# Kernel optimization log

Hardware: AMD Instinct MI355X
Metric: run time of the kernel (lower is better)

The kernel has to match this reference:

```python
import jax, jax.numpy as jnp
import numpy as np

GRID = (8, 8)
B, C, H, W = 16, 256, 64, 64
N_NETS = GRID[0] * GRID[1]
EPS = 1e-5  # torch BatchNorm2d default


def _region_index():
    # Faithful to the original code: networks[i * j + j] == networks[j*(i+1)]
    gh, gw = GRID
    i = np.arange(gh)[:, None]
    j = np.arange(gw)[None, :]
    return (i * j + j).reshape(-1)  # [gh*gw] int indices into the 64 networks


def setup_inputs() -> dict:
    key = jax.random.key(0)
    ks = jax.random.split(key, 7)
    x = jax.random.normal(ks[0], (B, C, H, W), jnp.float32)
    gamma = 1.0 + 0.1 * jax.random.normal(ks[1], (N_NETS, C), jnp.float32)
    beta = 0.1 * jax.random.normal(ks[2], (N_NETS, C), jnp.float32)
    mean = 0.1 * jax.random.normal(ks[3], (N_NETS, C), jnp.float32)
    var = jax.random.uniform(ks[4], (N_NETS, C), jnp.float32, minval=0.5, maxval=1.5)
    conv_w = 0.05 * jax.random.normal(ks[5], (N_NETS, C, C, 3, 3), jnp.float32)
    conv_b = 0.01 * jax.random.normal(ks[6], (N_NETS, C), jnp.float32)
    return dict(x=x, gamma=gamma, beta=beta, mean=mean, var=var,
                conv_w=conv_w, conv_b=conv_b)


def reference(x, gamma, beta, mean, var, conv_w, conv_b):
    gh, gw = GRID
    b, c, h, w = x.shape
    ph, pw = h // gh, w // gw
    # [B,C,H,W] -> [gh*gw, B, C, ph, pw]
    xp = (x.reshape(b, c, gh, ph, gw, pw)
           .transpose(2, 4, 0, 1, 3, 5)
           .reshape(gh * gw, b, c, ph, pw))

    idx = jnp.asarray(_region_index())
    g, bt, m, v = gamma[idx], beta[idx], mean[idx], var[idx]
    wk, cb = conv_w[idx], conv_b[idx]

    def region(xi, gi, bi, mi, vi, wi, cbi):
        # inference-mode BatchNorm2d
        scale = (gi * jax.lax.rsqrt(vi + EPS))[None, :, None, None]
        hh = (xi - mi[None, :, None, None]) * scale + bi[None, :, None, None]
        hh = jax.nn.relu(hh)
        y = jax.lax.conv_general_dilated(
            hh, wi, window_strides=(1, 1), padding=((1, 1), (1, 1)),
            dimension_numbers=('NCHW', 'OIHW', 'NCHW'))
        return y + cbi[None, :, None, None] + xi  # residual add

    yp = jax.vmap(region)(xp, g, bt, m, v, wk, cb)  # [gh*gw, B, C, ph, pw]
    y = (yp.reshape(gh, gw, b, c, ph, pw)
           .transpose(2, 3, 0, 4, 1, 5)
           .reshape(b, c, h, w))
    return y
```

## Files before the change

### kernel.cpp

```cpp
#include <hip/hip_runtime.h>
#include <hip/hip_bf16.h>
#include <stdint.h>


typedef __attribute__((ext_vector_type(8))) short bf16x8;
typedef __attribute__((ext_vector_type(4))) float f32x4;

typedef const __attribute__((address_space(1))) unsigned int gu32;
typedef __attribute__((address_space(3))) unsigned int lu32;

__device__ __forceinline__ void g2l16(const void* g, void* l) {
  __builtin_amdgcn_global_load_lds((gu32*)g, (lu32*)l, 16, 0, 0);
}

__device__ __forceinline__ unsigned short f2bf(float f) {
  union { __hip_bfloat16 h; unsigned short u; } cv;
  cv.h = __float2bfloat16(f);
  return cv.u;
}

__global__ void wtrans_kernel(const float* __restrict__ w,
                              __hip_bfloat16* __restrict__ wb) {
  const int co8 = blockIdx.x;
  const int net = blockIdx.y;
  const int tid = threadIdx.x;
  __shared__ __align__(16) unsigned short t[9 * 8 * 256];

  const int cip = tid & 127;
  const int ch  = tid >> 7;
  const int ci0 = cip * 2;

#pragma unroll
  for (int cl = 0; cl < 4; ++cl) {
    const int col = ch * 4 + cl;
    const int co = co8 * 8 + col;
    const float* src = w + ((size_t)(net * 256 + co) * 256 + ci0) * 9;
    float a[18];
#pragma unroll
    for (int i = 0; i < 18; ++i) a[i] = src[i];
#pragma unroll
    for (int tap = 0; tap < 9; ++tap) {
      unsigned int pk = (unsigned)f2bf(a[tap]) | ((unsigned)f2bf(a[tap + 9]) << 16);
      *(unsigned int*)&t[tap * 2048 + col * 256 + ci0] = pk;
    }
  }
  __syncthreads();

  __hip_bfloat16* base = wb + (size_t)net * 589824;
#pragma unroll
  for (int k = 0; k < 9; ++k) {
    int ck = k * 256 + tid;
    int tap = ck >> 8;
    int col = (ck >> 5) & 7;
    int cr = ck & 31;
    bf16x8 v = *(const bf16x8*)&t[tap * 2048 + col * 256 + cr * 8];
    unsigned short* dst = (unsigned short*)base +
        ((size_t)tap * 256 + co8 * 8 + col) * 256 + cr * 8;
    *(bf16x8*)dst = v;
  }
}

__global__ void bnrelu_kernel(const float* __restrict__ x,
                              const float* __restrict__ gamma,
                              const float* __restrict__ beta,
                              const float* __restrict__ mean,
                              const float* __restrict__ var,
                              __hip_bfloat16* __restrict__ hh) {
  const int blk = blockIdx.x;
  const int reg = blk >> 4, b = blk & 15;
  const int gi = reg >> 3, gj = reg & 7;
  const int net = gj * (gi + 1);
  const int tid = threadIdx.x;

  __shared__ float sc[256], sh[256];
  __shared__ __align__(16) unsigned short tile[64 * 256];

  {
    float g = gamma[net * 256 + tid];
    float bt = beta[net * 256 + tid];
    float m = mean[net * 256 + tid];
    float v = var[net * 256 + tid];
    float s = g * rsqrtf(v + 1e-5f);
    sc[tid] = s;
    sh[tid] = bt - m * s;
  }
  __syncthreads();

  const float* xb = x + (size_t)b * 1048576 + (gi * 8) * 64 + gj * 8;
  const int px = tid & 63, cw = tid >> 6;
  const int yy = px >> 3, xx = px & 7;

#pragma unroll
  for (int j = 0; j < 8; ++j) {
    const int chunk = cw * 8 + j;
    const int c0 = chunk * 8;
    bf16x8 v;
#pragma unroll
    for (int e = 0; e < 8; ++e) {
      int c = c0 + e;
      float tv = xb[(size_t)c * 4096 + yy * 64 + xx];
      tv = fmaxf(tv * sc[c] + sh[c], 0.f);
      v[e] = (short)f2bf(tv);
    }
    int phys = (chunk + px) & 31;
    *(bf16x8*)&tile[px * 256 + phys * 8] = v;
  }
  __syncthreads();

  unsigned short* hb = (unsigned short*)(hh + (size_t)(reg * 16 + b) * 16384);
#pragma unroll
  for (int k = 0; k < 8; ++k) {
    int ck = k * 256 + tid;
    int p = ck >> 5, cl = ck & 31;
    int phys = (cl + p) & 31;
    bf16x8 v = *(const bf16x8*)&tile[p * 256 + phys * 8];
    *(bf16x8*)(hb + p * 256 + cl * 8) = v;
  }
}

__global__ __launch_bounds__(256, 2) void conv_kernel(
    const __hip_bfloat16* __restrict__ hh,
    const __hip_bfloat16* __restrict__ wb,
    const float* __restrict__ xin,
    const float* __restrict__ cbias,
    float* __restrict__ outp) {
  __shared__ __align__(16) char sA[66048];

  const int bx = blockIdx.x;
  const int r = bx >> 4;
  const int mt = bx & 7;
  const int nt = (bx >> 3) & 1;
  const int gi = r >> 3, gj = r & 7;
  const int net = gj * (gi + 1);

  const int tid = threadIdx.x;
  const int lane = tid & 63;
  const int wv = tid >> 6;
  const int wm = (wv & 1) * 64;
  const int wn = (wv >> 1) * 64;
  const int ln = lane & 15;
  const int q = lane >> 4;

  const __hip_bfloat16* Aslab = hh + (size_t)(r * 16 + mt * 2) * (64 * 256);

#pragma unroll
  for (int i = 0; i < 16; ++i) {
    int s = i * 256 + tid;
    int row = s >> 5, sp = s & 31;
    int cl = (sp & 24) | (((sp & 7) - row) & 7);
    g2l16(Aslab + (size_t)row * 256 + cl * 8, sA + s * 16);
  }
  if (tid < 32) *(f32x4*)(sA + 65536 + tid * 16) = (f32x4){0.f, 0.f, 0.f, 0.f};
  __syncthreads();

  const unsigned short* Bl = (const unsigned short*)wb +
      (size_t)net * 589824 + (size_t)(nt * 128 + wn + ln) * 256 + q * 8;

  int bl[4], py[4], pxr[4];
#pragma unroll
  for (int mf = 0; mf < 4; ++mf) {
    int m = wm + mf * 16 + ln;
    bl[mf] = m >> 6;
    py[mf] = (m >> 3) & 7;
    pxr[mf] = m & 7;
  }

  f32x4 acc[4][4];
#pragma unroll
  for (int mf = 0; mf < 4; ++mf)
#pragma unroll
    for (int nf = 0; nf < 4; ++nf)
      acc[mf][nf] = (f32x4){0.f, 0.f, 0.f, 0.f};

#pragma unroll 1
  for (int cc = 0; cc < 4; ++cc) {
#pragma unroll
    for (int tap = 0; tap < 9; ++tap) {
      const int dy = tap / 3 - 1, dx = tap % 3 - 1;
      bf16x8 bfr[4][2];
#pragma unroll
      for (int nf = 0; nf < 4; ++nf)
#pragma unroll
        for (int kk = 0; kk < 2; ++kk)
          bfr[nf][kk] = *(const bf16x8*)(Bl + (size_t)tap * 65536 +
                                         nf * 4096 + cc * 64 + kk * 32);
      int arow[4];
#pragma unroll
      for (int mf = 0; mf < 4; ++mf) {
        int sy = py[mf] + dy, sx = pxr[mf] + dx;
        bool v = ((unsigned)sy < 8u) & ((unsigned)sx < 8u);
        arow[mf] = v ? (bl[mf] * 64 + sy * 8 + sx) : 128;
      }
#pragma unroll
      for (int kk = 0; kk < 2; ++kk) {
        bf16x8 afr[4];
#pragma unroll
        for (int mf = 0; mf < 4; ++mf) {
          int row = arow[mf];
          int phys = cc * 8 + ((kk * 4 + q + row) & 7);
          afr[mf] = *(const bf16x8*)(sA + row * 512 + phys * 16);
        }
#pragma unroll
        for (int mf = 0; mf < 4; ++mf)
#pragma unroll
          for (int nf = 0; nf < 4; ++nf)
            acc[mf][nf] = __builtin_amdgcn_mfma_f32_16x16x32_bf16(
                afr[mf], bfr[nf][kk], acc[mf][nf], 0, 0, 0);
      }
    }
  }

  const int nbase = nt * 128 + wn;
#pragma unroll
  for (int nf = 0; nf < 4; ++nf) {
    const int n = nbase + nf * 16 + ln;
    const float cb = cbias[net * 256 + n];
#pragma unroll
    for (int mf = 0; mf < 4; ++mf) {
      int mloc = wm + mf * 16 + q * 4;
      int b = mt * 2 + (mloc >> 6);
      int px = mloc & 63;
      int yy = px >> 3, x0 = px & 7;
      size_t off =
          (((size_t)b * 256 + n) * 64 + (gi * 8 + yy)) * 64 + (gj * 8 + x0);
      f32x4 res = *(const f32x4*)(xin + off);
      f32x4 o = acc[mf][nf];
      o = o + res;
      o = o + cb;
      *(f32x4*)(outp + off) = o;
    }
  }
}

extern "C" void kernel_launch(void* const* d_in, const int* in_sizes, int n_in,
                              void* d_out, int out_size, void* d_ws,
                              size_t ws_size, hipStream_t stream) {
  const float* x      = (const float*)d_in[0];
  const float* gamma  = (const float*)d_in[1];
  const float* beta   = (const float*)d_in[2];
  const float* mean   = (const float*)d_in[3];
  const float* var    = (const float*)d_in[4];
  const float* conv_w = (const float*)d_in[5];
  const float* conv_b = (const float*)d_in[6];
  float* out = (float*)d_out;

  __hip_bfloat16* wb = (__hip_bfloat16*)d_ws;
  __hip_bfloat16* hh = (__hip_bfloat16*)((char*)d_ws + 75497472);

  wtrans_kernel<<<dim3(32, 64), 256, 0, stream>>>(conv_w, wb);
  bnrelu_kernel<<<1024, 256, 0, stream>>>(x, gamma, beta, mean, var, hh);
  conv_kernel<<<1024, 256, 0, stream>>>(hh, wb, x, conv_b, out);
}
```

Baseline: 479.6 us.

## Enlarge conv tile to 256x256 with double-buffered LDS weight staging

The conv kernel now computes a 256-pixel by 256-output-channel tile per block, with 8x8 MFMA fragments per wave. Activations are staged per channel chunk and weight slices are double-buffered in LDS through global_load_lds, replacing the direct global weight loads. Out-of-bounds taps are masked with a zero select instead of a padding row. The weight transpose kernel now stages fp32 weights through LDS with async loads before converting. The trade-off is only 256 blocks at one block per CU, plus a heavy register footprint and a barrier per K step.

```diff
diff --git a/kernel.cpp b/kernel.cpp
--- a/kernel.cpp
+++ b/kernel.cpp
@@ -21,42 +21,36 @@
 
 __global__ void wtrans_kernel(const float* __restrict__ w,
                               __hip_bfloat16* __restrict__ wb) {
-  const int co8 = blockIdx.x;
+  const int cog = blockIdx.x;
   const int net = blockIdx.y;
   const int tid = threadIdx.x;
-  __shared__ __align__(16) unsigned short t[9 * 8 * 256];
-
-  const int cip = tid & 127;
-  const int ch  = tid >> 7;
-  const int ci0 = cip * 2;
-
-#pragma unroll
-  for (int cl = 0; cl < 4; ++cl) {
-    const int col = ch * 4 + cl;
-    const int co = co8 * 8 + col;
-    const float* src = w + ((size_t)(net * 256 + co) * 256 + ci0) * 9;
-    float a[18];
-#pragma unroll
-    for (int i = 0; i < 18; ++i) a[i] = src[i];
-#pragma unroll
-    for (int tap = 0; tap < 9; ++tap) {
-      unsigned int pk = (unsigned)f2bf(a[tap]) | ((unsigned)f2bf(a[tap + 9]) << 16);
-      *(unsigned int*)&t[tap * 2048 + col * 256 + ci0] = pk;
-    }
-  }
-  __syncthreads();
-
-  __hip_bfloat16* base = wb + (size_t)net * 589824;
-#pragma unroll
-  for (int k = 0; k < 9; ++k) {
-    int ck = k * 256 + tid;
-    int tap = ck >> 8;
-    int col = (ck >> 5) & 7;
-    int cr = ck & 31;
-    bf16x8 v = *(const bf16x8*)&t[tap * 2048 + col * 256 + cr * 8];
-    unsigned short* dst = (unsigned short*)base +
-        ((size_t)tap * 256 + co8 * 8 + col) * 256 + cr * 8;
-    *(bf16x8*)dst = v;
+  __shared__ __align__(16) float wsm[9216];
+
+  const float* src = w + ((size_t)net * 256 + cog * 4) * 2304;
+#pragma unroll
+  for (int p = 0; p < 9; ++p) {
+    int s = p * 256 + tid;
+    g2l16(src + s * 4, (char*)wsm + s * 16);
+  }
+  __syncthreads();
+
+  unsigned short* base = (unsigned short*)wb + (size_t)net * 589824;
+#pragma unroll
+  for (int it = 0; it < 5; ++it) {
+    int c = it * 256 + tid;
+    if (c < 1152) {
+      int cv = (c * 7282) >> 16;
+      int tap = c - cv * 9;
+      int co_l = cv >> 5;
+      int ci0 = (cv & 31) << 3;
+      int dbase = co_l * 2304 + ci0 * 9 + tap;
+      bf16x8 v;
+#pragma unroll
+      for (int e = 0; e < 8; ++e) v[e] = (short)f2bf(wsm[dbase + e * 9]);
+      unsigned short* dst =
+          base + ((size_t)(tap * 256 + cog * 4 + co_l) * 256 + ci0);
+      *(bf16x8*)dst = v;
+    }
   }
 }
 
@@ -118,107 +112,131 @@
   }
 }
 
-__global__ __launch_bounds__(256, 2) void conv_kernel(
+__global__ __launch_bounds__(256, 1) void conv_kernel(
     const __hip_bfloat16* __restrict__ hh,
     const __hip_bfloat16* __restrict__ wb,
     const float* __restrict__ xin,
     const float* __restrict__ cbias,
     float* __restrict__ outp) {
-  __shared__ __align__(16) char sA[66048];
+  __shared__ __align__(16) char sA[32768];
+  __shared__ __align__(16) char sB[32768];
 
   const int bx = blockIdx.x;
-  const int r = bx >> 4;
-  const int mt = bx & 7;
-  const int nt = (bx >> 3) & 1;
+  const int r = bx >> 2;
+  const int mq = bx & 3;
   const int gi = r >> 3, gj = r & 7;
   const int net = gj * (gi + 1);
 
   const int tid = threadIdx.x;
   const int lane = tid & 63;
   const int wv = tid >> 6;
-  const int wm = (wv & 1) * 64;
-  const int wn = (wv >> 1) * 64;
+  const int wm = (wv & 1) * 128;
+  const int wn = (wv >> 1) * 128;
   const int ln = lane & 15;
   const int q = lane >> 4;
 
-  const __hip_bfloat16* Aslab = hh + (size_t)(r * 16 + mt * 2) * (64 * 256);
-
-#pragma unroll
-  for (int i = 0; i < 16; ++i) {
-    int s = i * 256 + tid;
-    int row = s >> 5, sp = s & 31;
-    int cl = (sp & 24) | (((sp & 7) - row) & 7);
-    g2l16(Aslab + (size_t)row * 256 + cl * 8, sA + s * 16);
-  }
-  if (tid < 32) *(f32x4*)(sA + 65536 + tid * 16) = (f32x4){0.f, 0.f, 0.f, 0.f};
-  __syncthreads();
-
-  const unsigned short* Bl = (const unsigned short*)wb +
-      (size_t)net * 589824 + (size_t)(nt * 128 + wn + ln) * 256 + q * 8;
-
-  int bl[4], py[4], pxr[4];
-#pragma unroll
-  for (int mf = 0; mf < 4; ++mf) {
+  const unsigned short* hb =
+      (const unsigned short*)hh + (size_t)(r * 16 + mq * 4) * 16384;
+  const unsigned short* wbase = (const unsigned short*)wb + (size_t)net * 589824;
+
+  const int pxw = ln & 7;
+  int pyb[8], rowb[8];
+#pragma unroll
+  for (int mf = 0; mf < 8; ++mf) {
     int m = wm + mf * 16 + ln;
-    bl[mf] = m >> 6;
-    py[mf] = (m >> 3) & 7;
-    pxr[mf] = m & 7;
-  }
-
-  f32x4 acc[4][4];
-#pragma unroll
-  for (int mf = 0; mf < 4; ++mf)
-#pragma unroll
-    for (int nf = 0; nf < 4; ++nf)
-      acc[mf][nf] = (f32x4){0.f, 0.f, 0.f, 0.f};
-
+    pyb[mf] = (m >> 3) & 7;
+    rowb[mf] = m & 0xC0;
+  }
+  int boff[8];
+#pragma unroll
+  for (int nf = 0; nf < 8; ++nf) {
+    int row = wn + nf * 16 + ln;
+    boff[nf] = row * 64 + ((q + row) & 3) * 16;
+  }
+
+  f32x4 acc[8][8];
+#pragma unroll
+  for (int mf = 0; mf < 8; ++mf)
+#pragma unroll
+    for (int nf = 0; nf < 8; ++nf) acc[mf][nf] = (f32x4){0.f, 0.f, 0.f, 0.f};
+
+  const bf16x8 zero8 = {0, 0, 0, 0, 0, 0, 0, 0};
+
+  auto stageA = [&](int cc) {
+#pragma unroll
+    for (int p = 0; p < 8; ++p) {
+      int s = p * 256 + tid;
+      int row = s >> 3;
+      int lg = ((s & 7) - row) & 7;
+      g2l16(hb + (row >> 6) * 16384 + (row & 63) * 256 + cc * 64 + lg * 8,
+            sA + s * 16);
+    }
+  };
+  auto stageB = [&](int cc32, int tap, int buf) {
+#pragma unroll
+    for (int p = 0; p < 4; ++p) {
+      int s = p * 256 + tid;
+      int row = s >> 2;
+      int lg = ((s & 3) - row) & 3;
+      g2l16(wbase + (size_t)tap * 65536 + row * 256 + cc32 * 32 + lg * 8,
+            sB + buf * 16384 + s * 16);
+    }
+  };
+
+  stageA(0);
+  stageB(0, 0, 0);
+  __syncthreads();
+
+  int j = 0;
 #pragma unroll 1
   for (int cc = 0; cc < 4; ++cc) {
-#pragma unroll
-    for (int tap = 0; tap < 9; ++tap) {
-      const int dy = tap / 3 - 1, dx = tap % 3 - 1;
-      bf16x8 bfr[4][2];
-#pragma unroll
-      for (int nf = 0; nf < 4; ++nf)
-#pragma unroll
-        for (int kk = 0; kk < 2; ++kk)
-          bfr[nf][kk] = *(const bf16x8*)(Bl + (size_t)tap * 65536 +
-                                         nf * 4096 + cc * 64 + kk * 32);
-      int arow[4];
-#pragma unroll
-      for (int mf = 0; mf < 4; ++mf) {
-        int sy = py[mf] + dy, sx = pxr[mf] + dx;
-        bool v = ((unsigned)sy < 8u) & ((unsigned)sx < 8u);
-        arow[mf] = v ? (bl[mf] * 64 + sy * 8 + sx) : 128;
+#pragma unroll 1
+    for (int t = 0; t < 18; ++t, ++j) {
+      int jn = j + 1;
+      if (jn < 72) {
+        int ccn = (jn * 3641) >> 16;
+        int tn = jn - ccn * 18;
+        stageB(ccn * 2 + (tn & 1), tn >> 1, jn & 1);
       }
-#pragma unroll
-      for (int kk = 0; kk < 2; ++kk) {
-        bf16x8 afr[4];
-#pragma unroll
-        for (int mf = 0; mf < 4; ++mf) {
-          int row = arow[mf];
-          int phys = cc * 8 + ((kk * 4 + q + row) & 7);
-          afr[mf] = *(const bf16x8*)(sA + row * 512 + phys * 16);
-        }
-#pragma unroll
-        for (int mf = 0; mf < 4; ++mf)
-#pragma unroll
-          for (int nf = 0; nf < 4; ++nf)
-            acc[mf][nf] = __builtin_amdgcn_mfma_f32_16x16x32_bf16(
-                afr[mf], bfr[nf][kk], acc[mf][nf], 0, 0, 0);
+      const int tap = t >> 1, h = t & 1;
+      const int tp3 = (tap * 11) >> 5;
+      const int dy = tp3 - 1, dx = tap - tp3 * 3 - 1;
+      const char* bbuf = sB + (j & 1) * 16384;
+
+      bf16x8 bfr[8];
+#pragma unroll
+      for (int nf = 0; nf < 8; ++nf)
+        bfr[nf] = *(const bf16x8*)(bbuf + boff[nf]);
+
+#pragma unroll
+      for (int mf = 0; mf < 8; ++mf) {
+        int sy = pyb[mf] + dy, sx = pxw + dx;
+        bool ok = ((unsigned)sy < 8u) & ((unsigned)sx < 8u);
+        int row = rowb[mf] | ((sy & 7) << 3) | (sx & 7);
+        int ph = (h * 4 + q + row) & 7;
+        bf16x8 a = *(const bf16x8*)(sA + row * 128 + ph * 16);
+        a = ok ? a : zero8;
+#pragma unroll
+        for (int nf = 0; nf < 8; ++nf)
+          acc[mf][nf] = __builtin_amdgcn_mfma_f32_16x16x32_bf16(
+              a, bfr[nf], acc[mf][nf], 0, 0, 0);
       }
-    }
-  }
-
-  const int nbase = nt * 128 + wn;
-#pragma unroll
-  for (int nf = 0; nf < 4; ++nf) {
-    const int n = nbase + nf * 16 + ln;
+      __syncthreads();
+      if (t == 17 && cc < 3) {
+        stageA(cc + 1);
+        __syncthreads();
+      }
+    }
+  }
+
+#pragma unroll
+  for (int nf = 0; nf < 8; ++nf) {
+    const int n = wn + nf * 16 + ln;
     const float cb = cbias[net * 256 + n];
 #pragma unroll
-    for (int mf = 0; mf < 4; ++mf) {
+    for (int mf = 0; mf < 8; ++mf) {
       int mloc = wm + mf * 16 + q * 4;
-      int b = mt * 2 + (mloc >> 6);
+      int b = mq * 4 + (mloc >> 6);
       int px = mloc & 63;
       int yy = px >> 3, x0 = px & 7;
       size_t off =
@@ -247,7 +265,7 @@
   __hip_bfloat16* wb = (__hip_bfloat16*)d_ws;
   __hip_bfloat16* hh = (__hip_bfloat16*)((char*)d_ws + 75497472);
 
-  wtrans_kernel<<<dim3(32, 64), 256, 0, stream>>>(conv_w, wb);
+  wtrans_kernel<<<dim3(64, 64), 256, 0, stream>>>(conv_w, wb);
   bnrelu_kernel<<<1024, 256, 0, stream>>>(x, gamma, beta, mean, var, hh);
-  conv_kernel<<<1024, 256, 0, stream>>>(hh, wb, x, conv_b, out);
-}
+  conv_kernel<<<256, 256, 0, stream>>>(hh, wb, x, conv_b, out);
+}
```

After: 443.4 us. -7.5%, faster.
